# Performance work log

Hardware: AMD Instinct MI355X
Metric: run time of the kernel (lower is better)

The kernel has to match this reference:

```python
import jax, jax.numpy as jnp
import numpy as np


def _checkerboard(shape):
    idx = np.indices(shape).sum(axis=0)
    return jnp.asarray(1 - idx % 2, dtype=jnp.float32)


def _to_patches(z, p):
    # einops: 'b c (h p1) (w p2) -> b (h w) (c p1 p2)'
    B, C, H, W = z.shape
    h, w = H // p, W // p
    return z.reshape(B, C, h, p, w, p).transpose(0, 2, 4, 1, 3, 5).reshape(B, h * w, C * p * p)


def _from_patches(x, p, shape):
    # inverse of _to_patches (matches reverse_rearrange row-major patch placement)
    B, C, H, W = shape
    h, w = H // p, W // p
    return x.reshape(B, h, w, C, p, p).transpose(0, 3, 1, 4, 2, 5).reshape(B, C, H, W)


def setup_inputs() -> dict:
    key = jax.random.key(0)
    kx, kq, kk = jax.random.split(key, 3)
    B, C, H, W = 32, 96, 128, 128
    x = jax.random.normal(kx, (B, C, H, W), dtype=jnp.float32)
    # kaiming_uniform_(a=sqrt(5)) on [C,C,1,1]: bound = sqrt(6/((1+5)*fan_in)) = 1/sqrt(C)
    bound = 1.0 / np.sqrt(C)
    convq = jax.random.uniform(kq, (C, C), dtype=jnp.float32, minval=-bound, maxval=bound)
    convk = jax.random.uniform(kk, (C, C), dtype=jnp.float32, minval=-bound, maxval=bound)
    offset = jnp.array([0.99], dtype=jnp.float32)
    offset2 = jnp.array([8.0], dtype=jnp.float32)
    offset3 = jnp.array([0.001], dtype=jnp.float32)
    return {"input": x, "convq": convq, "convk": convk,
            "offset": offset, "offset2": offset2, "offset3": offset3}


def reference(input, convq, convk, offset, offset2, offset3):
    x = input
    B, C, H, W = x.shape
    p = W // 2                      # patch = half the image -> always 4 patches (2x2)
    D = C * p * p
    full_inp = _to_patches(x, p)    # [B, 4, D]
    mask = _checkerboard((4, D))    # elementwise checkerboard over (patch, feature)
    f_m = full_inp * mask
    z_m = _from_patches(f_m, p, x.shape)          # masked image
    # 1x1 convs == channel mixing
    q = jnp.einsum('bchw,oc->bohw', z_m, convq)
    k = jnp.einsum('bchw,oc->bohw', z_m, convk)
    fq = _to_patches(q, p)          # [B, 4, D]
    fk = _to_patches(k, p)
    am = _checkerboard((4, 4))
    scores = jnp.einsum('bnd,bmd->bnm', fq, fk)   # [B, 4, 4]
    attn = (jax.nn.leaky_relu(scores + offset2, negative_slope=1e-4) + offset3) * am
    # the m1/m2 gather + offset*eye(2) + scatter-back in the original is equivalent
    # to adding offset on the full diagonal (diag positions are at even parity)
    attn = attn + offset * jnp.eye(4, dtype=x.dtype)
    m1 = attn[:, 0::2, 0::2]        # even-parity rows/cols -> [B, 2, 2]
    m2 = attn[:, 1::2, 1::2]        # odd-parity rows/cols  -> [B, 2, 2]
    scale = p * (p // 2) * C
    logdet = (jnp.linalg.slogdet(m1)[1] + jnp.linalg.slogdet(m2)[1]) * scale  # [B]
    out = jnp.einsum('bnm,bmd->bnd', attn, full_inp * (1.0 - mask))
    out_final = out * (1.0 - mask) + full_inp * mask
    output = _from_patches(out_final, p, x.shape)
    return output, logdet
```

## Files before the change

### kernel.cpp

```cpp
#include <hip/hip_runtime.h>

typedef float  f32x4  __attribute__((ext_vector_type(4)));
typedef short  bf16x8 __attribute__((ext_vector_type(8)));

#define HWI    16384
#define IMG    (96*16384)
#define NPIX   50331648

#define WS_G   0
#define WS_SP  16384

__device__ __forceinline__ unsigned short f2bf(float f){
    unsigned u = __builtin_bit_cast(unsigned, f);
    u += 0x7fffu + ((u >> 16) & 1u);
    return (unsigned short)(u >> 16);
}

__global__ void kG(const float* __restrict__ cq, const float* __restrict__ ck,
                   float* __restrict__ G){
    int idx = blockIdx.x * 256 + threadIdx.x;
    if (idx >= 9216) return;
    int c = idx / 96, cp = idx - c * 96;
    float s = 0.f;
    #pragma unroll 8
    for (int o = 0; o < 96; ++o) s += cq[o*96 + c] * ck[o*96 + cp];
    G[idx] = s;
}

__launch_bounds__(384, 3)
__global__ void kM(const float* __restrict__ x, const float* __restrict__ G,
                   float* __restrict__ sp){
    const int blk = blockIdx.x;
    const int b = blk >> 4, wp = (blk >> 3) & 1, ks = blk & 7;
    const int tid = threadIdx.x;
    const int wave = tid >> 6, lane = tid & 63;
    const int q  = wave >> 1;
    const int h  = wave & 1;
    const int qr = (q == 2) ? 1 : 0;
    const int qc = (q == 0) ? 0 : 1;

    __shared__ unsigned short Zs[2][192][40];

    f32x4 acc[3][6];
    #pragma unroll
    for (int a = 0; a < 3; ++a)
      #pragma unroll
      for (int b2 = 0; b2 < 6; ++b2)
        acc[a][b2] = (f32x4){0.f, 0.f, 0.f, 0.f};

    const int l16 = tid & 15, rr = tid >> 4;
    const float* xb = x + (size_t)b * IMG + wp * 64 + l16 * 4;
    const int frow = lane & 15, fko = (lane >> 4) << 3;

    f32x4 v[8];
    {
        const int i0 = ks * 8;
        #pragma unroll
        for (int p = 0; p < 8; ++p){
            const int row = rr + p * 24;
            const int cch = (row < 96) ? row : row - 96;
            const int hh  = (row < 96) ? i0  : i0 + 64;
            v[p] = *(const f32x4*)(xb + (size_t)cch * HWI + hh * 128);
        }
    }

    for (int step = 0; step < 8; ++step){
        const int cur = step & 1;
        #pragma unroll
        for (int p = 0; p < 8; ++p){
            const int row = rr + p * 24;
            unsigned pk = (wp == 0)
                ? ((unsigned)f2bf(v[p][0]) | ((unsigned)f2bf(v[p][2]) << 16))
                : ((unsigned)f2bf(v[p][1]) | ((unsigned)f2bf(v[p][3]) << 16));
            *(unsigned*)(&Zs[cur][row][l16 * 2]) = pk;
        }
        __syncthreads();
        if (step < 7){
            const int i = ks * 8 + step + 1;
            #pragma unroll
            for (int p = 0; p < 8; ++p){
                const int row = rr + p * 24;
                const int cch = (row < 96) ? row : row - 96;
                const int hh  = (row < 96) ? i   : i + 64;
                v[p] = *(const f32x4*)(xb + (size_t)cch * HWI + hh * 128);
            }
        }
        bf16x8 af[3], bfv[6];
        #pragma unroll
        for (int t3 = 0; t3 < 3; ++t3)
            af[t3] = *(const bf16x8*)(&Zs[cur][qr*96 + (h*3 + t3)*16 + frow][fko]);
        #pragma unroll
        for (int t6 = 0; t6 < 6; ++t6)
            bfv[t6] = *(const bf16x8*)(&Zs[cur][qc*96 + t6*16 + frow][fko]);
        #pragma unroll
        for (int tr = 0; tr < 3; ++tr)
          #pragma unroll
          for (int tc = 0; tc < 6; ++tc)
            acc[tr][tc] = __builtin_amdgcn_mfma_f32_16x16x32_bf16(
                              af[tr], bfv[tc], acc[tr][tc], 0, 0, 0);
    }

    const int r0 = (lane >> 4) * 4, c0 = lane & 15;
    float p0 = 0.f, p1 = 0.f;
    #pragma unroll
    for (int tr = 0; tr < 3; ++tr){
      #pragma unroll
      for (int tc = 0; tc < 6; ++tc){
        #pragma unroll
        for (int e = 0; e < 4; ++e){
          const int R = (h*3 + tr)*16 + r0 + e;
          const int C = tc*16 + c0;
          const float m = acc[tr][tc][e];
          p0 += G[R*96 + C] * m;
          if (q == 1) p1 += G[C*96 + R] * m;
        }
      }
    }
    #pragma unroll
    for (int off = 32; off > 0; off >>= 1){
        p0 += __shfl_down(p0, off, 64);
        if (q == 1) p1 += __shfl_down(p1, off, 64);
    }
    if (lane == 0){
        float* s = sp + (size_t)blk * 8;
        s[wave] = p0;
        if (q == 1) s[6 + h] = p1;
    }
}

__launch_bounds__(256)
__global__ void kOut(const float* __restrict__ x, const float* __restrict__ sp,
                     const float* __restrict__ o1p, const float* __restrict__ o2p,
                     const float* __restrict__ o3p, float* __restrict__ out){
    __shared__ float A[2][4];
    const int blk = blockIdx.x, tid = threadIdx.x;
    const int r = blk >> 3;
    const int b = r / 96;

    if (tid < 8){
        const int wp = tid >> 2, comp = tid & 3;
        const int s0 = (comp == 0) ? 0 : (comp == 1) ? 2 : (comp == 2) ? 6 : 4;
        const float* base = sp + (size_t)((b*2 + wp) * 8) * 8;
        float s = 0.f;
        #pragma unroll
        for (int ks = 0; ks < 8; ++ks) s += base[ks*8 + s0] + base[ks*8 + s0 + 1];
        s += o2p[0];
        s = (s >= 0.f ? s : 1e-4f * s) + o3p[0];
        if (comp == 0 || comp == 3) s += o1p[0];
        A[wp][comp] = s;
    }
    __syncthreads();

    if (tid == 8 && (blk % 768) == 0){
        float ld = logf(fabsf(A[0][0]*A[0][3] - A[0][1]*A[0][2]))
                 + logf(fabsf(A[1][0]*A[1][3] - A[1][1]*A[1][2]));
        out[NPIX + b] = ld * 196608.0f;
    }

    const int idx = blk * 256 + tid;
    const int wq = idx & 31;
    const int i  = (idx >> 5) & 63;
    const size_t base = ((size_t)r * 128 + i) * 128 + wq * 4;
    f32x4 top = *(const f32x4*)(x + base);
    f32x4 bot = *(const f32x4*)(x + base + 8192);
    const int wp = wq >> 4;
    const float a00 = A[wp][0], a01 = A[wp][1], a10 = A[wp][2], a11 = A[wp][3];
    f32x4 ot, ob;
    #pragma unroll
    for (int e = 0; e < 4; ++e){
        const bool mix = ((wp + e) & 1) != 0;
        ot[e] = mix ? (a00 * top[e] + a01 * bot[e]) : top[e];
        ob[e] = mix ? (a10 * top[e] + a11 * bot[e]) : bot[e];
    }
    __builtin_nontemporal_store(ot, (f32x4*)(out + base));
    __builtin_nontemporal_store(ob, (f32x4*)(out + base + 8192));
}

extern "C" void kernel_launch(void* const* d_in, const int* in_sizes, int n_in,
                              void* d_out, int out_size, void* d_ws, size_t ws_size,
                              hipStream_t stream){
    const float* x  = (const float*)d_in[0];
    const float* cq = (const float*)d_in[1];
    const float* ck = (const float*)d_in[2];
    const float* o1 = (const float*)d_in[3];
    const float* o2 = (const float*)d_in[4];
    const float* o3 = (const float*)d_in[5];
    float* out = (float*)d_out;
    float* ws  = (float*)d_ws;

    kG  <<<36, 256, 0, stream>>>(cq, ck, ws + WS_G);
    kM  <<<512, 384, 0, stream>>>(x, ws + WS_G, ws + WS_SP);
    kOut<<<24576, 256, 0, stream>>>(x, ws + WS_SP, o1, o2, o3, out);
}
```

Measured before the change: 107.8 us.

## Fuse Gram, scores and output passes into one persistent kernel with atomic flags

```diff
diff --git a/kernel.cpp b/kernel.cpp
--- a/kernel.cpp
+++ b/kernel.cpp
@@ -9,6 +9,10 @@
 
 #define WS_G   0
 #define WS_SP  16384
+#define WS_A   20480
+#define WS_CTR 20736
+
+#define SPIN_MAX (1 << 22)
 
 __device__ __forceinline__ unsigned short f2bf(float f){
     unsigned u = __builtin_bit_cast(unsigned, f);
@@ -16,20 +20,31 @@
     return (unsigned short)(u >> 16);
 }
 
-__global__ void kG(const float* __restrict__ cq, const float* __restrict__ ck,
-                   float* __restrict__ G){
-    int idx = blockIdx.x * 256 + threadIdx.x;
-    if (idx >= 9216) return;
-    int c = idx / 96, cp = idx - c * 96;
+__device__ __forceinline__ float attn_comp(const float* __restrict__ sp, int b, int w2,
+                                           int comp, float o1, float o2, float o3){
+    const int s0 = (comp == 0) ? 0 : (comp == 1) ? 2 : (comp == 2) ? 6 : 4;
+    const float* base = sp + (size_t)((b*2 + w2) * 8) * 8;
     float s = 0.f;
-    #pragma unroll 8
-    for (int o = 0; o < 96; ++o) s += cq[o*96 + c] * ck[o*96 + cp];
-    G[idx] = s;
+    #pragma unroll
+    for (int k2 = 0; k2 < 8; ++k2) s += base[k2*8 + s0] + base[k2*8 + s0 + 1];
+    s += o2;
+    s = (s >= 0.f ? s : 1e-4f * s) + o3;
+    if (comp == 0 || comp == 3) s += o1;
+    return s;
 }
 
 __launch_bounds__(384, 3)
-__global__ void kM(const float* __restrict__ x, const float* __restrict__ G,
-                   float* __restrict__ sp){
+__global__ void kFused(const float* __restrict__ x, const float* __restrict__ cq,
+                       const float* __restrict__ ck, float* __restrict__ ws,
+                       const float* __restrict__ o1p, const float* __restrict__ o2p,
+                       const float* __restrict__ o3p, float* __restrict__ out)
+{
+    float* G    = ws + WS_G;
+    float* sp   = ws + WS_SP;
+    float* Aws  = ws + WS_A;
+    int*   ci   = (int*)(ws + WS_CTR);
+    int*   gcnt = ci;
+
     const int blk = blockIdx.x;
     const int b = blk >> 4, wp = (blk >> 3) & 1, ks = blk & 7;
     const int tid = threadIdx.x;
@@ -39,7 +54,26 @@
     const int qr = (q == 2) ? 1 : 0;
     const int qc = (q == 0) ? 0 : 1;
 
+    int* bcnt_b  = ci + 16  + b * 16;
+    int* aflag_b = ci + 528 + b * 16;
+
     __shared__ unsigned short Zs[2][192][40];
+    __shared__ float As8[8];
+    __shared__ int   isLast;
+
+    if (blk < 24){
+        const int idx = blk * 384 + tid;
+        const int c = idx / 96, cp = idx - c * 96;
+        float s = 0.f;
+        #pragma unroll 8
+        for (int o = 0; o < 96; ++o) s += cq[o*96 + c] * ck[o*96 + cp];
+        G[idx] = s;
+        __syncthreads();
+        if (tid == 0){
+            __threadfence();
+            __hip_atomic_fetch_add(gcnt, 1, __ATOMIC_RELEASE, __HIP_MEMORY_SCOPE_AGENT);
+        }
+    }
 
     f32x4 acc[3][6];
     #pragma unroll
@@ -100,80 +134,114 @@
                               af[tr], bfv[tc], acc[tr][tc], 0, 0, 0);
     }
 
-    const int r0 = (lane >> 4) * 4, c0 = lane & 15;
-    float p0 = 0.f, p1 = 0.f;
-    #pragma unroll
-    for (int tr = 0; tr < 3; ++tr){
-      #pragma unroll
-      for (int tc = 0; tc < 6; ++tc){
-        #pragma unroll
-        for (int e = 0; e < 4; ++e){
-          const int R = (h*3 + tr)*16 + r0 + e;
-          const int C = tc*16 + c0;
-          const float m = acc[tr][tc][e];
-          p0 += G[R*96 + C] * m;
-          if (q == 1) p1 += G[C*96 + R] * m;
-        }
-      }
-    }
-    #pragma unroll
-    for (int off = 32; off > 0; off >>= 1){
-        p0 += __shfl_down(p0, off, 64);
-        if (q == 1) p1 += __shfl_down(p1, off, 64);
-    }
-    if (lane == 0){
-        float* s = sp + (size_t)blk * 8;
-        s[wave] = p0;
-        if (q == 1) s[6 + h] = p1;
-    }
-}
-
-__launch_bounds__(256)
-__global__ void kOut(const float* __restrict__ x, const float* __restrict__ sp,
-                     const float* __restrict__ o1p, const float* __restrict__ o2p,
-                     const float* __restrict__ o3p, float* __restrict__ out){
-    __shared__ float A[2][4];
-    const int blk = blockIdx.x, tid = threadIdx.x;
-    const int r = blk >> 3;
-    const int b = r / 96;
-
-    if (tid < 8){
-        const int wp = tid >> 2, comp = tid & 3;
-        const int s0 = (comp == 0) ? 0 : (comp == 1) ? 2 : (comp == 2) ? 6 : 4;
-        const float* base = sp + (size_t)((b*2 + wp) * 8) * 8;
-        float s = 0.f;
-        #pragma unroll
-        for (int ks = 0; ks < 8; ++ks) s += base[ks*8 + s0] + base[ks*8 + s0 + 1];
-        s += o2p[0];
-        s = (s >= 0.f ? s : 1e-4f * s) + o3p[0];
-        if (comp == 0 || comp == 3) s += o1p[0];
-        A[wp][comp] = s;
-    }
-    __syncthreads();
-
-    if (tid == 8 && (blk % 768) == 0){
-        float ld = logf(fabsf(A[0][0]*A[0][3] - A[0][1]*A[0][2]))
-                 + logf(fabsf(A[1][0]*A[1][3] - A[1][1]*A[1][2]));
-        out[NPIX + b] = ld * 196608.0f;
-    }
-
-    const int idx = blk * 256 + tid;
-    const int wq = idx & 31;
-    const int i  = (idx >> 5) & 63;
-    const size_t base = ((size_t)r * 128 + i) * 128 + wq * 4;
-    f32x4 top = *(const f32x4*)(x + base);
-    f32x4 bot = *(const f32x4*)(x + base + 8192);
-    const int wp = wq >> 4;
-    const float a00 = A[wp][0], a01 = A[wp][1], a10 = A[wp][2], a11 = A[wp][3];
-    f32x4 ot, ob;
-    #pragma unroll
-    for (int e = 0; e < 4; ++e){
-        const bool mix = ((wp + e) & 1) != 0;
-        ot[e] = mix ? (a00 * top[e] + a01 * bot[e]) : top[e];
-        ob[e] = mix ? (a10 * top[e] + a11 * bot[e]) : bot[e];
-    }
-    __builtin_nontemporal_store(ot, (f32x4*)(out + base));
-    __builtin_nontemporal_store(ob, (f32x4*)(out + base + 8192));
+    if (tid == 0){
+        int it = 0;
+        while (__hip_atomic_load(gcnt, __ATOMIC_ACQUIRE, __HIP_MEMORY_SCOPE_AGENT) < 24
+               && it < SPIN_MAX){ __builtin_amdgcn_s_sleep(1); ++it; }
+        __threadfence();
+    }
+    __syncthreads();
+
+    {
+        const int r0 = (lane >> 4) * 4, c0 = lane & 15;
+        float p0 = 0.f, p1 = 0.f;
+        #pragma unroll
+        for (int tr = 0; tr < 3; ++tr){
+          #pragma unroll
+          for (int tc = 0; tc < 6; ++tc){
+            #pragma unroll
+            for (int e = 0; e < 4; ++e){
+              const int R = (h*3 + tr)*16 + r0 + e;
+              const int C = tc*16 + c0;
+              const float m = acc[tr][tc][e];
+              p0 += G[R*96 + C] * m;
+              if (q == 1) p1 += G[C*96 + R] * m;
+            }
+          }
+        }
+        #pragma unroll
+        for (int off = 32; off > 0; off >>= 1){
+            p0 += __shfl_down(p0, off, 64);
+            if (q == 1) p1 += __shfl_down(p1, off, 64);
+        }
+        if (lane == 0){
+            float* s = sp + (size_t)blk * 8;
+            s[wave] = p0;
+            if (q == 1) s[6 + h] = p1;
+        }
+    }
+    __syncthreads();
+
+    const float o1 = o1p[0], o2 = o2p[0], o3 = o3p[0];
+    if (tid == 0){
+        __threadfence();
+        int prev = __hip_atomic_fetch_add(bcnt_b, 1, __ATOMIC_ACQ_REL,
+                                          __HIP_MEMORY_SCOPE_AGENT);
+        isLast = (prev == 15);
+        if (prev == 15) __threadfence();
+    }
+    __syncthreads();
+    if (isLast){
+        if (tid < 8){
+            const int w2 = tid >> 2, comp = tid & 3;
+            As8[tid] = attn_comp(sp, b, w2, comp, o1, o2, o3);
+        }
+        __syncthreads();
+        if (tid == 0){
+            const float d0 = As8[0]*As8[3] - As8[1]*As8[2];
+            const float d1 = As8[4]*As8[7] - As8[5]*As8[6];
+            out[NPIX + b] = (logf(fabsf(d0)) + logf(fabsf(d1))) * 196608.0f;
+            #pragma unroll
+            for (int i2 = 0; i2 < 8; ++i2) Aws[b*8 + i2] = As8[i2];
+            __threadfence();
+            __hip_atomic_store(aflag_b, 1, __ATOMIC_RELEASE, __HIP_MEMORY_SCOPE_AGENT);
+        }
+    }
+
+    if (tid == 0){
+        int it = 0;
+        while (__hip_atomic_load(aflag_b, __ATOMIC_ACQUIRE, __HIP_MEMORY_SCOPE_AGENT) == 0
+               && it < SPIN_MAX){ __builtin_amdgcn_s_sleep(1); ++it; }
+        __threadfence();
+    }
+    __syncthreads();
+
+    const float a00 = __hip_atomic_load(Aws + b*8 + wp*4 + 0, __ATOMIC_RELAXED, __HIP_MEMORY_SCOPE_AGENT);
+    const float a01 = __hip_atomic_load(Aws + b*8 + wp*4 + 1, __ATOMIC_RELAXED, __HIP_MEMORY_SCOPE_AGENT);
+    const float a10 = __hip_atomic_load(Aws + b*8 + wp*4 + 2, __ATOMIC_RELAXED, __HIP_MEMORY_SCOPE_AGENT);
+    const float a11 = __hip_atomic_load(Aws + b*8 + wp*4 + 3, __ATOMIC_RELAXED, __HIP_MEMORY_SCOPE_AGENT);
+
+    const float* xb2 = x   + (size_t)b * IMG + wp * 64;
+    float*       ob2 = out + (size_t)b * IMG + wp * 64;
+
+    #pragma unroll 1
+    for (int g2 = 0; g2 < 8; ++g2){
+        f32x4 tv[4], bv[4];
+        int offs[4];
+        #pragma unroll
+        for (int u = 0; u < 4; ++u){
+            const int pi  = (g2*4 + u)*384 + tid;
+            const int ch  = pi >> 7;
+            const int rem = pi & 127;
+            const int row = 7 - (rem >> 4);
+            const int cv  = rem & 15;
+            offs[u] = ch * HWI + (ks*8 + row) * 128 + cv * 4;
+            tv[u] = *(const f32x4*)(xb2 + offs[u]);
+            bv[u] = *(const f32x4*)(xb2 + offs[u] + 8192);
+        }
+        #pragma unroll
+        for (int u = 0; u < 4; ++u){
+            f32x4 ot, ob;
+            #pragma unroll
+            for (int e = 0; e < 4; ++e){
+                const bool mix = ((wp + e) & 1) != 0;
+                ot[e] = mix ? (a00 * tv[u][e] + a01 * bv[u][e]) : tv[u][e];
+                ob[e] = mix ? (a10 * tv[u][e] + a11 * bv[u][e]) : bv[u][e];
+            }
+            __builtin_nontemporal_store(ot, (f32x4*)(ob2 + offs[u]));
+            __builtin_nontemporal_store(ob, (f32x4*)(ob2 + offs[u] + 8192));
+        }
+    }
 }
 
 extern "C" void kernel_launch(void* const* d_in, const int* in_sizes, int n_in,
@@ -188,7 +256,6 @@
     float* out = (float*)d_out;
     float* ws  = (float*)d_ws;
 
-    kG  <<<36, 256, 0, stream>>>(cq, ck, ws + WS_G);
-    kM  <<<512, 384, 0, stream>>>(x, ws + WS_G, ws + WS_SP);
-    kOut<<<24576, 256, 0, stream>>>(x, ws + WS_SP, o1, o2, o3, out);
-}
+    hipMemsetAsync((void*)(ws + WS_CTR), 0, 1040 * sizeof(int), stream);
+    kFused<<<512, 384, 0, stream>>>(x, cq, ck, ws, o1, o2, o3, out);
+}
```

Measured after the change: 182.6 us. +69.4%, slower.

## Fuse Gram-matrix compute into kM and finalize attention via last-block atomic

Applied to the files above, without the earlier changes.

```diff
diff --git a/kernel.cpp b/kernel.cpp
--- a/kernel.cpp
+++ b/kernel.cpp
@@ -7,8 +7,9 @@
 #define IMG    (96*16384)
 #define NPIX   50331648
 
-#define WS_G   0
 #define WS_SP  16384
+#define WS_A   20480
+#define WS_CTR 20736
 
 __device__ __forceinline__ unsigned short f2bf(float f){
     unsigned u = __builtin_bit_cast(unsigned, f);
@@ -16,20 +17,29 @@
     return (unsigned short)(u >> 16);
 }
 
-__global__ void kG(const float* __restrict__ cq, const float* __restrict__ ck,
-                   float* __restrict__ G){
-    int idx = blockIdx.x * 256 + threadIdx.x;
-    if (idx >= 9216) return;
-    int c = idx / 96, cp = idx - c * 96;
+__device__ __forceinline__ float attn_comp(const float* __restrict__ sp, int b, int w2,
+                                           int comp, float o1, float o2, float o3){
+    const int s0 = (comp == 0) ? 0 : (comp == 1) ? 2 : (comp == 2) ? 6 : 4;
+    const float* base = sp + (size_t)((b*2 + w2) * 8) * 8;
     float s = 0.f;
-    #pragma unroll 8
-    for (int o = 0; o < 96; ++o) s += cq[o*96 + c] * ck[o*96 + cp];
-    G[idx] = s;
+    #pragma unroll
+    for (int k2 = 0; k2 < 8; ++k2) s += base[k2*8 + s0] + base[k2*8 + s0 + 1];
+    s += o2;
+    s = (s >= 0.f ? s : 1e-4f * s) + o3;
+    if (comp == 0 || comp == 3) s += o1;
+    return s;
 }
 
 __launch_bounds__(384, 3)
-__global__ void kM(const float* __restrict__ x, const float* __restrict__ G,
-                   float* __restrict__ sp){
+__global__ void kM(const float* __restrict__ x, const float* __restrict__ cq,
+                   const float* __restrict__ ck, float* __restrict__ ws,
+                   const float* __restrict__ o1p, const float* __restrict__ o2p,
+                   const float* __restrict__ o3p, float* __restrict__ out)
+{
+    float* sp  = ws + WS_SP;
+    float* Aws = ws + WS_A;
+    int*   ci  = (int*)(ws + WS_CTR);
+
     const int blk = blockIdx.x;
     const int b = blk >> 4, wp = (blk >> 3) & 1, ks = blk & 7;
     const int tid = threadIdx.x;
@@ -39,7 +49,14 @@
     const int qr = (q == 2) ? 1 : 0;
     const int qc = (q == 0) ? 0 : 1;
 
-    __shared__ unsigned short Zs[2][192][40];
+    int* bcnt_b = ci + b * 16;
+
+    __shared__ __align__(16) unsigned char shraw[36864];
+    typedef unsigned short ZsT[192][40];
+    ZsT*   Zs = (ZsT*)shraw;
+    float* Gs = (float*)shraw;
+    __shared__ float As8[8];
+    __shared__ int   isLast;
 
     f32x4 acc[3][6];
     #pragma unroll
@@ -100,62 +117,90 @@
                               af[tr], bfv[tc], acc[tr][tc], 0, 0, 0);
     }
 
-    const int r0 = (lane >> 4) * 4, c0 = lane & 15;
-    float p0 = 0.f, p1 = 0.f;
-    #pragma unroll
-    for (int tr = 0; tr < 3; ++tr){
-      #pragma unroll
-      for (int tc = 0; tc < 6; ++tc){
-        #pragma unroll
-        for (int e = 0; e < 4; ++e){
-          const int R = (h*3 + tr)*16 + r0 + e;
-          const int C = tc*16 + c0;
-          const float m = acc[tr][tc][e];
-          p0 += G[R*96 + C] * m;
-          if (q == 1) p1 += G[C*96 + R] * m;
-        }
-      }
-    }
-    #pragma unroll
-    for (int off = 32; off > 0; off >>= 1){
-        p0 += __shfl_down(p0, off, 64);
-        if (q == 1) p1 += __shfl_down(p1, off, 64);
-    }
-    if (lane == 0){
-        float* s = sp + (size_t)blk * 8;
-        s[wave] = p0;
-        if (q == 1) s[6 + h] = p1;
+    __syncthreads();
+    {
+        const int c = tid >> 2, cp0 = (tid & 3) * 24;
+        f32x4 s4[6];
+        #pragma unroll
+        for (int j = 0; j < 6; ++j) s4[j] = (f32x4){0.f, 0.f, 0.f, 0.f};
+        for (int o = 0; o < 96; ++o){
+            const float a = cq[o*96 + c];
+            const f32x4* ckr = (const f32x4*)(ck + o*96 + cp0);
+            #pragma unroll
+            for (int j = 0; j < 6; ++j){
+                const f32x4 cv = ckr[j];
+                s4[j][0] += a * cv[0]; s4[j][1] += a * cv[1];
+                s4[j][2] += a * cv[2]; s4[j][3] += a * cv[3];
+            }
+        }
+        #pragma unroll
+        for (int j = 0; j < 6; ++j)
+            *(f32x4*)(Gs + c*96 + cp0 + j*4) = s4[j];
+    }
+    __syncthreads();
+
+    {
+        const int r0 = (lane >> 4) * 4, c0 = lane & 15;
+        float p0 = 0.f, p1 = 0.f;
+        #pragma unroll
+        for (int tr = 0; tr < 3; ++tr){
+          #pragma unroll
+          for (int tc = 0; tc < 6; ++tc){
+            #pragma unroll
+            for (int e = 0; e < 4; ++e){
+              const int R = (h*3 + tr)*16 + r0 + e;
+              const int C = tc*16 + c0;
+              const float m = acc[tr][tc][e];
+              p0 += Gs[R*96 + C] * m;
+              if (q == 1) p1 += Gs[C*96 + R] * m;
+            }
+          }
+        }
+        #pragma unroll
+        for (int off = 32; off > 0; off >>= 1){
+            p0 += __shfl_down(p0, off, 64);
+            if (q == 1) p1 += __shfl_down(p1, off, 64);
+        }
+        if (lane == 0){
+            float* s = sp + (size_t)blk * 8;
+            s[wave] = p0;
+            if (q == 1) s[6 + h] = p1;
+        }
+    }
+    __syncthreads();
+
+    if (tid == 0){
+        __threadfence();
+        int prev = __hip_atomic_fetch_add(bcnt_b, 1, __ATOMIC_ACQ_REL,
+                                          __HIP_MEMORY_SCOPE_AGENT);
+        isLast = (prev == 15);
+        if (prev == 15) __threadfence();
+    }
+    __syncthreads();
+    if (isLast){
+        if (tid < 8){
+            As8[tid] = attn_comp(sp, b, tid >> 2, tid & 3, o1p[0], o2p[0], o3p[0]);
+            Aws[b*8 + tid] = As8[tid];
+        }
+        __syncthreads();
+        if (tid == 0){
+            const float d0 = As8[0]*As8[3] - As8[1]*As8[2];
+            const float d1 = As8[4]*As8[7] - As8[5]*As8[6];
+            out[NPIX + b] = (logf(fabsf(d0)) + logf(fabsf(d1))) * 196608.0f;
+        }
     }
 }
 
 __launch_bounds__(256)
-__global__ void kOut(const float* __restrict__ x, const float* __restrict__ sp,
-                     const float* __restrict__ o1p, const float* __restrict__ o2p,
-                     const float* __restrict__ o3p, float* __restrict__ out){
-    __shared__ float A[2][4];
+__global__ void kOut(const float* __restrict__ x, const float* __restrict__ Aws,
+                     float* __restrict__ out){
+    __shared__ float A[8];
     const int blk = blockIdx.x, tid = threadIdx.x;
     const int r = blk >> 3;
     const int b = r / 96;
 
-    if (tid < 8){
-        const int wp = tid >> 2, comp = tid & 3;
-        const int s0 = (comp == 0) ? 0 : (comp == 1) ? 2 : (comp == 2) ? 6 : 4;
-        const float* base = sp + (size_t)((b*2 + wp) * 8) * 8;
-        float s = 0.f;
-        #pragma unroll
-        for (int ks = 0; ks < 8; ++ks) s += base[ks*8 + s0] + base[ks*8 + s0 + 1];
-        s += o2p[0];
-        s = (s >= 0.f ? s : 1e-4f * s) + o3p[0];
-        if (comp == 0 || comp == 3) s += o1p[0];
-        A[wp][comp] = s;
-    }
-    __syncthreads();
-
-    if (tid == 8 && (blk % 768) == 0){
-        float ld = logf(fabsf(A[0][0]*A[0][3] - A[0][1]*A[0][2]))
-                 + logf(fabsf(A[1][0]*A[1][3] - A[1][1]*A[1][2]));
-        out[NPIX + b] = ld * 196608.0f;
-    }
+    if (tid < 8) A[tid] = Aws[b*8 + tid];
+    __syncthreads();
 
     const int idx = blk * 256 + tid;
     const int wq = idx & 31;
@@ -164,7 +209,7 @@
     f32x4 top = *(const f32x4*)(x + base);
     f32x4 bot = *(const f32x4*)(x + base + 8192);
     const int wp = wq >> 4;
-    const float a00 = A[wp][0], a01 = A[wp][1], a10 = A[wp][2], a11 = A[wp][3];
+    const float a00 = A[wp*4+0], a01 = A[wp*4+1], a10 = A[wp*4+2], a11 = A[wp*4+3];
     f32x4 ot, ob;
     #pragma unroll
     for (int e = 0; e < 4; ++e){
@@ -188,7 +233,7 @@
     float* out = (float*)d_out;
     float* ws  = (float*)d_ws;
 
-    kG  <<<36, 256, 0, stream>>>(cq, ck, ws + WS_G);
-    kM  <<<512, 384, 0, stream>>>(x, ws + WS_G, ws + WS_SP);
-    kOut<<<24576, 256, 0, stream>>>(x, ws + WS_SP, o1, o2, o3, out);
-}
+    hipMemsetAsync((void*)(ws + WS_CTR), 0, 32 * 16 * sizeof(int), stream);
+    kM  <<<512, 384, 0, stream>>>(x, cq, ck, ws, o1, o2, o3, out);
+    kOut<<<24576, 256, 0, stream>>>(x, ws + WS_A, out);
+}
```

New measurement: 207.5 us. 1.92x slower.

## Double-register prefetch in kM with explicit LDS-only barrier

Applied to the files above, without the earlier changes.

```diff
diff --git a/kernel.cpp b/kernel.cpp
--- a/kernel.cpp
+++ b/kernel.cpp
@@ -51,54 +51,66 @@
     const int l16 = tid & 15, rr = tid >> 4;
     const float* xb = x + (size_t)b * IMG + wp * 64 + l16 * 4;
     const int frow = lane & 15, fko = (lane >> 4) << 3;
-
-    f32x4 v[8];
-    {
-        const int i0 = ks * 8;
-        #pragma unroll
-        for (int p = 0; p < 8; ++p){
-            const int row = rr + p * 24;
-            const int cch = (row < 96) ? row : row - 96;
-            const int hh  = (row < 96) ? i0  : i0 + 64;
-            v[p] = *(const f32x4*)(xb + (size_t)cch * HWI + hh * 128);
-        }
-    }
-
-    for (int step = 0; step < 8; ++step){
-        const int cur = step & 1;
-        #pragma unroll
-        for (int p = 0; p < 8; ++p){
-            const int row = rr + p * 24;
-            unsigned pk = (wp == 0)
-                ? ((unsigned)f2bf(v[p][0]) | ((unsigned)f2bf(v[p][2]) << 16))
-                : ((unsigned)f2bf(v[p][1]) | ((unsigned)f2bf(v[p][3]) << 16));
-            *(unsigned*)(&Zs[cur][row][l16 * 2]) = pk;
-        }
-        __syncthreads();
-        if (step < 7){
-            const int i = ks * 8 + step + 1;
-            #pragma unroll
-            for (int p = 0; p < 8; ++p){
-                const int row = rr + p * 24;
-                const int cch = (row < 96) ? row : row - 96;
-                const int hh  = (row < 96) ? i   : i + 64;
-                v[p] = *(const f32x4*)(xb + (size_t)cch * HWI + hh * 128);
-            }
-        }
-        bf16x8 af[3], bfv[6];
-        #pragma unroll
-        for (int t3 = 0; t3 < 3; ++t3)
-            af[t3] = *(const bf16x8*)(&Zs[cur][qr*96 + (h*3 + t3)*16 + frow][fko]);
-        #pragma unroll
-        for (int t6 = 0; t6 < 6; ++t6)
-            bfv[t6] = *(const bf16x8*)(&Zs[cur][qc*96 + t6*16 + frow][fko]);
-        #pragma unroll
-        for (int tr = 0; tr < 3; ++tr)
-          #pragma unroll
-          for (int tc = 0; tc < 6; ++tc)
-            acc[tr][tc] = __builtin_amdgcn_mfma_f32_16x16x32_bf16(
-                              af[tr], bfv[tc], acc[tr][tc], 0, 0, 0);
-    }
+    const int i0 = ks * 8;
+
+    #define BARRIER_LGKM() asm volatile("s_waitcnt lgkmcnt(0)\ns_barrier" ::: "memory")
+
+    #define LOADR(dst, ii) do { \
+        _Pragma("unroll") \
+        for (int p = 0; p < 8; ++p){ \
+            const int row_ = rr + p * 24; \
+            const int cch_ = (row_ < 96) ? row_ : row_ - 96; \
+            const int hh_  = (row_ < 96) ? (ii) : (ii) + 64; \
+            dst[p] = *(const f32x4*)(xb + (size_t)cch_ * HWI + hh_ * 128); \
+        } } while(0)
+
+    #define PACK(src, bufc) do { \
+        _Pragma("unroll") \
+        for (int p = 0; p < 8; ++p){ \
+            const int row_ = rr + p * 24; \
+            unsigned pk_ = (wp == 0) \
+                ? ((unsigned)f2bf(src[p][0]) | ((unsigned)f2bf(src[p][2]) << 16)) \
+                : ((unsigned)f2bf(src[p][1]) | ((unsigned)f2bf(src[p][3]) << 16)); \
+            *(unsigned*)(&Zs[bufc][row_][l16 * 2]) = pk_; \
+        } } while(0)
+
+    #define FRAG_MFMA(bufc) do { \
+        bf16x8 af[3], bfv[6]; \
+        _Pragma("unroll") \
+        for (int t3 = 0; t3 < 3; ++t3) \
+            af[t3] = *(const bf16x8*)(&Zs[bufc][qr*96 + (h*3 + t3)*16 + frow][fko]); \
+        _Pragma("unroll") \
+        for (int t6 = 0; t6 < 6; ++t6) \
+            bfv[t6] = *(const bf16x8*)(&Zs[bufc][qc*96 + t6*16 + frow][fko]); \
+        _Pragma("unroll") \
+        for (int tr = 0; tr < 3; ++tr) \
+          _Pragma("unroll") \
+          for (int tc = 0; tc < 6; ++tc) \
+            acc[tr][tc] = __builtin_amdgcn_mfma_f32_16x16x32_bf16( \
+                              af[tr], bfv[tc], acc[tr][tc], 0, 0, 0); \
+        } while(0)
+
+    f32x4 v0[8], v1[8];
+    LOADR(v0, i0 + 0);
+    LOADR(v1, i0 + 1);
+
+    #pragma unroll 1
+    for (int it = 0; it < 4; ++it){
+        const int s0 = it * 2;
+        PACK(v0, 0);
+        BARRIER_LGKM();
+        if (s0 < 6) LOADR(v0, i0 + s0 + 2);
+        FRAG_MFMA(0);
+        PACK(v1, 1);
+        BARRIER_LGKM();
+        if (s0 < 5) LOADR(v1, i0 + s0 + 3);
+        FRAG_MFMA(1);
+    }
+
+    #undef BARRIER_LGKM
+    #undef LOADR
+    #undef PACK
+    #undef FRAG_MFMA
 
     const int r0 = (lane >> 4) * 4, c0 = lane & 15;
     float p0 = 0.f, p1 = 0.f;
```

Measured after the change: 128.5 us. 19.2% more time.
